# Kernel tuning notes

Hardware: AMD Instinct MI355X
Metric: run time of the kernel (lower is better)

The kernel has to match this reference:

```python
import jax, jax.numpy as jnp
import numpy as np

B, S, D = 4, 4096, 1024
H, DK, DV = 8, 128, 128
SEG = 512
DH = 4096
EPS = 1e-5


def setup_inputs() -> dict:
    key = jax.random.key(0)
    ks = jax.random.split(key, 8)
    n = lambda k, shp, sc: (jax.random.normal(k, shp, jnp.float32) * sc)
    return {
        "x": n(ks[0], (B, S, D), 1.0),
        "ln_gamma": jnp.ones((D,), jnp.float32),
        "ln_beta": jnp.zeros((D,), jnp.float32),
        "Wq": n(ks[1], (D, H * DK), 0.02),
        "Wk": n(ks[2], (D, H * DK), 0.02),
        "Wv": n(ks[3], (D, H * DV), 0.02),
        "Wo": n(ks[4], (H * DV, D), 0.02),
        "betas": n(ks[5], (1, H, 1, DV), 1.0),
        "ff_w1": n(ks[6], (D, DH), 0.02),
        "ff_b1": jnp.zeros((DH,), jnp.float32),
        "ff_w2": n(ks[7], (DH, D), 0.02),
        "ff_b2": jnp.zeros((D,), jnp.float32),
    }


def layer_norm(x, gamma, beta):
    mu = x.mean(-1, keepdims=True)
    var = x.var(-1, keepdims=True)
    return (x - mu) * jax.lax.rsqrt(var + EPS) * gamma + beta


def gelu_tanh(x):
    c = np.sqrt(2.0 / np.pi).astype(np.float32)
    return 0.5 * x * (1.0 + jnp.tanh(c * (x + 0.044715 * x * x * x)))


def infini_attention(x, Wq, Wk, Wv, Wo, betas):
    b, s, _ = x.shape
    nseg = s // SEG

    def proj(W, dh):
        # (b,s,H*dh) -> (nseg, b, H, SEG, dh)
        y = (x @ W).reshape(b, nseg, SEG, H, dh)
        return y.transpose(1, 0, 3, 2, 4)

    q = proj(Wq, DK)
    k = proj(Wk, DK)
    v = proj(Wv, DV)

    gate = jax.nn.sigmoid(betas)  # (1,H,1,DV)
    scale = 1.0 / np.sqrt(DK).astype(np.float32)
    causal_mask = jnp.tril(jnp.ones((SEG, SEG), bool))

    def step(carry, qkv):
        mem, z = carry  # (b,H,DK,DV), (b,H,DK,1)
        qs, ks_, vs = qkv  # (b,H,SEG,dk/dv)
        sq = jax.nn.elu(qs) + 1.0
        # compressive-memory retrieval
        att_mem = (sq @ mem) / (sq @ z)  # (b,H,SEG,DV)
        # local (segment) dot-product attention
        scores = jnp.einsum("bhqk,bhsk->bhqs", qs, ks_) * scale
        scores = jnp.where(causal_mask, scores, -jnp.inf)
        att = jax.nn.softmax(scores, axis=-1) @ vs  # (b,H,SEG,DV)
        # linear memory update
        sk = jax.nn.elu(ks_) + 1.0
        mem = mem + jnp.einsum("bhsk,bhsv->bhkv", sk, vs)
        z = z + sk.sum(axis=2)[..., None]
        out = gate * att_mem + (1.0 - gate) * att
        return (mem, z), out

    mem0 = jnp.zeros((b, H, DK, DV), x.dtype)
    z0 = jnp.ones((b, H, DK, 1), x.dtype) / DK
    _, outs = jax.lax.scan(step, (mem0, z0), (q, k, v))
    # (nseg,b,H,SEG,DV) -> (b,s,H*DV)
    outs = outs.transpose(1, 0, 3, 2, 4).reshape(b, s, H * DV)
    return outs @ Wo


def reference(x, ln_gamma, ln_beta, Wq, Wk, Wv, Wo, betas, ff_w1, ff_b1, ff_w2, ff_b2):
    h = layer_norm(x, ln_gamma, ln_beta)
    x = x + infini_attention(h, Wq, Wk, Wv, Wo, betas)
    h = layer_norm(x, ln_gamma, ln_beta)
    ff = gelu_tanh(h @ ff_w1 + ff_b1) @ ff_w2 + ff_b2
    return x + ff
```

## Files before the change

kernel.cpp:

```cpp
#include <hip/hip_runtime.h>

typedef unsigned short u16;
typedef unsigned int   u32;
typedef float f32x4 __attribute__((ext_vector_type(4)));
typedef short bf16x8 __attribute__((ext_vector_type(8)));

#define DEV static __device__ __forceinline__

DEV u16 f2b(float f){
  u32 u = __builtin_bit_cast(u32, f);
  return (u16)((u + 0x7fffu + ((u >> 16) & 1u)) >> 16);
}
DEV float b2f(u16 h){ u32 u = ((u32)h) << 16; return __builtin_bit_cast(float, u); }
DEV u32 pack2(float a, float b){ return (u32)f2b(a) | ((u32)f2b(b) << 16); }
DEV uint4 pack8(const float* f){
  uint4 r; r.x = pack2(f[0],f[1]); r.y = pack2(f[2],f[3]);
  r.z = pack2(f[4],f[5]); r.w = pack2(f[6],f[7]); return r;
}
DEV void unpack8(uint4 u, float* f){
  f[0]=b2f((u16)(u.x&0xffffu)); f[1]=b2f((u16)(u.x>>16));
  f[2]=b2f((u16)(u.y&0xffffu)); f[3]=b2f((u16)(u.y>>16));
  f[4]=b2f((u16)(u.z&0xffffu)); f[5]=b2f((u16)(u.z>>16));
  f[6]=b2f((u16)(u.w&0xffffu)); f[7]=b2f((u16)(u.w>>16));
}
DEV float gelu_t(float x){
  return 0.5f*x*(1.f + tanhf(0.7978845608028654f*(x + 0.044715f*x*x*x)));
}
DEV void g2l16(const u16* g, u16* l){
  __builtin_amdgcn_global_load_lds(
    (const __attribute__((address_space(1))) u32*)g,
    (__attribute__((address_space(3))) u32*)l, 16, 0, 0);
}

__global__ __launch_bounds__(256)
void ln_k(const float* __restrict__ x, const float* __restrict__ gamma,
          const float* __restrict__ beta, u16* __restrict__ out)
{
  const int row = blockIdx.x;
  const int t = threadIdx.x;
  const float4 v = ((const float4*)(x + (size_t)row*1024))[t];
  float s  = v.x+v.y+v.z+v.w;
  float ss = v.x*v.x+v.y*v.y+v.z*v.z+v.w*v.w;
  #pragma unroll
  for (int o=32;o;o>>=1){ s += __shfl_xor(s,o); ss += __shfl_xor(ss,o); }
  __shared__ float rs[4], rq[4];
  if ((t&63)==0){ rs[t>>6]=s; rq[t>>6]=ss; }
  __syncthreads();
  s  = rs[0]+rs[1]+rs[2]+rs[3];
  ss = rq[0]+rq[1]+rq[2]+rq[3];
  const float mean = s*(1.f/1024.f);
  const float var  = ss*(1.f/1024.f) - mean*mean;
  const float inv  = rsqrtf(var + 1e-5f);
  const float4 g4 = ((const float4*)gamma)[t];
  const float4 b4 = ((const float4*)beta)[t];
  float o[4];
  o[0]=(v.x-mean)*inv*g4.x+b4.x; o[1]=(v.y-mean)*inv*g4.y+b4.y;
  o[2]=(v.z-mean)*inv*g4.z+b4.z; o[3]=(v.w-mean)*inv*g4.w+b4.w;
  uint2 w; w.x = pack2(o[0],o[1]); w.y = pack2(o[2],o[3]);
  *(uint2*)(out + (size_t)row*1024 + t*4) = w;
}

__global__ __launch_bounds__(256)
void wconv_k(const float* __restrict__ W, u16* __restrict__ WT, int K, int N)
{
  __shared__ float tile[32][33];
  const int k0 = blockIdx.y<<5, n0 = blockIdx.x<<5;
  const int tx = threadIdx.x & 31, ty = threadIdx.x >> 5;
  #pragma unroll
  for (int r=0;r<32;r+=8)
    tile[ty+r][tx] = W[(size_t)(k0+ty+r)*N + n0+tx];
  __syncthreads();
  #pragma unroll
  for (int r=0;r<32;r+=8)
    WT[(size_t)(n0+ty+r)*K + k0+tx] = f2b(tile[tx][ty+r]);
}

#define EPI_QKV  0
#define EPI_WO   1
#define EPI_GELU 2
#define EPI_FF2  3

template<int EPI>
__global__ __launch_bounds__(512)
void gemm3_k(const u16* __restrict__ A, const u16* __restrict__ BT,
             int K, int lda, int ldb, int N,
             u16* __restrict__ obf, float* __restrict__ of32,
             const float* __restrict__ res, const float* __restrict__ bias)
{
  __shared__ __align__(16) u16 SA[2*4096];
  __shared__ __align__(16) u16 SB[2*8192];
  const int t = threadIdx.x, wid = t>>6, lane = t&63;
  const int c = lane&15, g = lane>>4;
  const int wm = wid>>2, wn = wid&3;
  const int nwg = gridDim.x*gridDim.y;
  const int lb = blockIdx.y*gridDim.x + blockIdx.x;
  const int nl = (lb&7)*(nwg>>3) + (lb>>3);
  const int bx = nl % gridDim.x, by = nl / gridDim.x;
  const int m0 = by<<7, n0 = bx<<8;
  const int srow = lane>>2;
  const int scol = (lane&3)<<3;
  const int sxor = (srow&3)<<3;
  const int rowA = (wid<<4) + srow;
  const u16* aSrc  = A  + (size_t)(m0 + rowA)*lda + (scol ^ sxor);
  const u16* bSrc0 = BT + (size_t)(n0 + rowA)*ldb + (scol ^ sxor);
  const u16* bSrc1 = BT + (size_t)(n0 + 128 + rowA)*ldb + (scol ^ sxor);
  const int kx = (g<<3) ^ ((c&3)<<3);

  f32x4 acc[4][4];
  const f32x4 zz = {0.f,0.f,0.f,0.f};
  #pragma unroll
  for (int i=0;i<4;i++){ acc[i][0]=zz; acc[i][1]=zz; acc[i][2]=zz; acc[i][3]=zz; }

  g2l16(aSrc,  &SA[wid<<9]);
  g2l16(bSrc0, &SB[wid<<9]);
  g2l16(bSrc1, &SB[(wid<<9) + 4096]);
  __syncthreads();

  const int nt = K >> 5;
  for (int tt = 0; tt < nt; ++tt){
    const int cur = tt & 1;
    if (tt + 1 < nt){
      const int ko = (tt+1) << 5;
      g2l16(aSrc + ko,  &SA[((cur^1)<<12) + (wid<<9)]);
      g2l16(bSrc0 + ko, &SB[((cur^1)<<13) + (wid<<9)]);
      g2l16(bSrc1 + ko, &SB[((cur^1)<<13) + (wid<<9) + 4096]);
    }
    bf16x8 af[4], bf[4];
    #pragma unroll
    for (int i=0;i<4;i++)
      af[i] = *(const bf16x8*)&SA[(cur<<12) + ((wm<<6)+(i<<4)+c)*32 + kx];
    #pragma unroll
    for (int j=0;j<4;j++)
      bf[j] = *(const bf16x8*)&SB[(cur<<13) + ((wn<<6)+(j<<4)+c)*32 + kx];
    #pragma unroll
    for (int i=0;i<4;i++)
      #pragma unroll
      for (int j=0;j<4;j++)
        acc[i][j] = __builtin_amdgcn_mfma_f32_16x16x32_bf16(af[i], bf[j], acc[i][j], 0,0,0);
    __syncthreads();
  }

  #pragma unroll
  for (int i=0;i<4;i++){
    const int gr0 = m0 + (wm<<6) + (i<<4) + (g<<2);
    #pragma unroll
    for (int j=0;j<4;j++){
      const int gc = n0 + (wn<<6) + (j<<4) + c;
      #pragma unroll
      for (int r=0;r<4;r++){
        const int gr = gr0 + r;
        const float vv = acc[i][j][r];
        if (EPI==EPI_QKV){
          obf[((size_t)(gc>>10)<<24) + (size_t)gr*1024 + (gc&1023)] = f2b(vv);
        } else if (EPI==EPI_WO){
          const size_t idx = (size_t)gr*N + gc;
          of32[idx] = res[idx] + vv;
        } else if (EPI==EPI_GELU){
          obf[(size_t)gr*N + gc] = f2b(gelu_t(vv + bias[gc]));
        } else {
          const size_t idx = (size_t)gr*N + gc;
          of32[idx] = of32[idx] + vv + (bias ? bias[gc] : 0.f);
        }
      }
    }
  }
}

__global__ __launch_bounds__(256)
void memseg_k(const u16* __restrict__ kb, const u16* __restrict__ vb,
              float* __restrict__ Mseg, float* __restrict__ zseg)
{
  const int bid = blockIdx.x;
  const int seg = bid & 7, h = (bid>>3)&7, b = bid>>6;
  __shared__ __align__(16) u16 Kt[128*64];
  __shared__ __align__(16) u16 Vt[128*64];
  const int t=threadIdx.x, w=t>>6, lane=t&63, c=lane&15, g=lane>>4;

  f32x4 acc[2][8];
  f32x4 zacc[2];
  const f32x4 zzero = {0.f,0.f,0.f,0.f};
  #pragma unroll
  for (int d=0;d<2;d++){ zacc[d]=zzero;
    #pragma unroll
    for (int j=0;j<8;j++) acc[d][j]=zzero; }
  bf16x8 bones;
  { u16 tmp[8];
    #pragma unroll
    for (int e=0;e<8;e++) tmp[e] = (c==0) ? (u16)0x3F80 : (u16)0;
    bones = __builtin_bit_cast(bf16x8, *(uint4*)tmp); }

  for (int s0=0; s0<512; s0+=64){
    __syncthreads();
    {
      const int s = lane, dk0 = w<<5;
      const size_t grow = ((size_t)b*4096 + seg*512 + s0 + s)*1024 + h*128 + dk0;
      #pragma unroll
      for (int jj=0;jj<4;jj++){
        float kf[8], vf[8];
        unpack8(*(const uint4*)(kb + grow + jj*8), kf);
        unpack8(*(const uint4*)(vb + grow + jj*8), vf);
        #pragma unroll
        for (int e=0;e<8;e++){
          const int dk = dk0 + jj*8 + e;
          const float ek = kf[e]>0.f ? kf[e]+1.f : __expf(kf[e]);
          Kt[(dk<<6) + (s ^ ((dk&7)<<3))] = f2b(ek);
          Vt[(dk<<6) + (s ^ ((dk&7)<<3))] = f2b(vf[e]);
        }
      }
    }
    __syncthreads();
    #pragma unroll
    for (int ks=0;ks<2;ks++){
      const int kc = (ks<<5) + (g<<3);
      const bf16x8 a0 = *(const bf16x8*)&Kt[((((w<<1)  )*16 + c)<<6) + (kc ^ ((c&7)<<3))];
      const bf16x8 a1 = *(const bf16x8*)&Kt[((((w<<1)+1)*16 + c)<<6) + (kc ^ ((c&7)<<3))];
      zacc[0] = __builtin_amdgcn_mfma_f32_16x16x32_bf16(a0, bones, zacc[0], 0,0,0);
      zacc[1] = __builtin_amdgcn_mfma_f32_16x16x32_bf16(a1, bones, zacc[1], 0,0,0);
      #pragma unroll
      for (int j=0;j<8;j++){
        const bf16x8 bv = *(const bf16x8*)&Vt[(((j<<4) + c)<<6) + (kc ^ ((c&7)<<3))];
        acc[0][j] = __builtin_amdgcn_mfma_f32_16x16x32_bf16(a0, bv, acc[0][j], 0,0,0);
        acc[1][j] = __builtin_amdgcn_mfma_f32_16x16x32_bf16(a1, bv, acc[1][j], 0,0,0);
      }
    }
  }
  const size_t mb = (size_t)bid*16384;
  #pragma unroll
  for (int d=0;d<2;d++){
    const int dk = ((w<<1)+d)*16 + (g<<2);
    #pragma unroll
    for (int j=0;j<8;j++)
      #pragma unroll
      for (int r=0;r<4;r++)
        Mseg[mb + (size_t)(dk + r)*128 + (j<<4) + c] = acc[d][j][r];
    if (c==0){
      #pragma unroll
      for (int r=0;r<4;r++) zseg[(size_t)bid*128 + dk + r] = zacc[d][r];
    }
  }
}

__global__ __launch_bounds__(256)
void scan_k(const float* __restrict__ Mseg, const float* __restrict__ zseg,
            u16* __restrict__ memBT, float* __restrict__ zB)
{
  const int bh = blockIdx.x >> 3, oct = blockIdx.x & 7;
  const int t = threadIdx.x;
  const int dv = (oct<<4) + (t&15);
  const int kd0 = (t>>4)<<3;
  float run[8];
  #pragma unroll
  for (int i=0;i<8;i++) run[i]=0.f;
  for (int seg=0; seg<8; seg++){
    const size_t base = ((size_t)bh*8 + seg)*16384;
    u16 tmp[8];
    #pragma unroll
    for (int i=0;i<8;i++) tmp[i] = f2b(run[i]);
    *(uint4*)(memBT + base + (size_t)dv*128 + kd0) = *(const uint4*)tmp;
    #pragma unroll
    for (int i=0;i<8;i++) run[i] += Mseg[base + (size_t)(kd0+i)*128 + dv];
  }
  if (oct==0 && t < 128){
    float zr = 1.f/128.f;
    for (int seg=0; seg<8; seg++){
      const size_t base = ((size_t)bh*8 + seg)*128;
      zB[base + t] = zr;
      zr += zseg[base + t];
    }
  }
}

__global__ __launch_bounds__(256,4)
void attn_k(const u16* __restrict__ qb, const u16* __restrict__ kb,
            const u16* __restrict__ vb, const u16* __restrict__ memBT,
            const float* __restrict__ zB, const float* __restrict__ betas,
            u16* __restrict__ attc)
{
  const int bid = blockIdx.x;
  const int s = bid & 255, rt = 7 - (bid >> 8);
  const int seg = s&7, h=(s>>3)&7, b=s>>6;
  __shared__ __align__(16) u16 smem[16384];
  __shared__ __align__(16) u16 Ps[4096];
  u16* Ks = smem;
  u16* Vt = smem + 8192;
  float* zP = (float*)Ps;
  const int t=threadIdx.x, w=t>>6, lane=t&63, c=lane&15, g=lane>>4;
  const size_t base = ((size_t)b*4096 + seg*512)*1024 + h*128;

  bf16x8 af[4];
  {
    const u16* qsrc = qb + base + (size_t)(rt*64 + (w<<4) + c)*1024 + (g<<3);
    #pragma unroll
    for (int ks=0;ks<4;ks++) af[ks] = *(const bf16x8*)(qsrc + ks*32);
  }
  f32x4 acc[8];
  #pragma unroll
  for (int f=0;f<8;f++) acc[f] = (f32x4){0.f,0.f,0.f,0.f};
  float m_run[4], l_run[4];
  #pragma unroll
  for (int r=0;r<4;r++){ m_run[r] = -1e30f; l_run[r] = 0.f; }
  const float scl = 0.08838834764831845f;

  for (int kc=0; kc<=rt; kc++){
    __syncthreads();
    #pragma unroll
    for (int j=0;j<4;j++){
      const int row = (j<<2) + (lane>>4);
      const u16* src = kb + base + (size_t)(kc*64 + (w<<4) + row)*1024
                       + ((size_t)((lane&15) ^ (((w<<4)+row)&7)) << 3);
      g2l16(src, Ks + (((w<<4)+(j<<2))<<7));
    }
    {
      const int kr = lane, d0 = w<<5;
      const u16* vsrc = vb + base + (size_t)(kc*64+kr)*1024 + d0;
      #pragma unroll
      for (int jj=0;jj<4;jj++){
        const uint4 vv = *(const uint4*)(vsrc + jj*8);
        u16 tmp[8]; *(uint4*)tmp = vv;
        #pragma unroll
        for (int e=0;e<8;e++){
          const int dv = d0 + jj*8 + e;
          Vt[(dv<<6) + (kr ^ ((dv&7)<<3))] = tmp[e];
        }
      }
    }
    __syncthreads();
    f32x4 sv[4];
    #pragma unroll
    for (int j=0;j<4;j++) sv[j] = (f32x4){0.f,0.f,0.f,0.f};
    #pragma unroll
    for (int ks=0;ks<4;ks++)
      #pragma unroll
      for (int j=0;j<4;j++){
        const bf16x8 bk = *(const bf16x8*)&Ks[(((j<<4)+c)<<7) + ((((ks<<2)|g) ^ (c&7))<<3)];
        sv[j] = __builtin_amdgcn_mfma_f32_16x16x32_bf16(af[ks], bk, sv[j], 0,0,0);
      }
    const bool diag = (kc==rt);
    float p[4][4], rm[4], rsum[4];
    #pragma unroll
    for (int r=0;r<4;r++){
      float mx = -1e30f;
      #pragma unroll
      for (int j=0;j<4;j++){
        float svv = sv[j][r]*scl;
        if (diag && ((j<<4)+c) > ((w<<4) + (g<<2) + r)) svv = -1e30f;
        p[j][r] = svv;
        mx = fmaxf(mx, svv);
      }
      rm[r] = mx;
    }
    #pragma unroll
    for (int o=1;o<16;o<<=1)
      #pragma unroll
      for (int r=0;r<4;r++) rm[r] = fmaxf(rm[r], __shfl_xor(rm[r], o));
    #pragma unroll
    for (int r=0;r<4;r++){
      const float mn = fmaxf(m_run[r], rm[r]);
      const float sc = __expf(m_run[r] - mn);
      m_run[r] = mn;
      float sum = 0.f;
      #pragma unroll
      for (int j=0;j<4;j++){ p[j][r] = __expf(p[j][r]-mn); sum += p[j][r]; }
      rsum[r] = sum;
      l_run[r] *= sc;
      #pragma unroll
      for (int f=0;f<8;f++) acc[f][r] *= sc;
    }
    #pragma unroll
    for (int o=1;o<16;o<<=1)
      #pragma unroll
      for (int r=0;r<4;r++) rsum[r] += __shfl_xor(rsum[r], o);
    #pragma unroll
    for (int r=0;r<4;r++) l_run[r] += rsum[r];
    #pragma unroll
    for (int j=0;j<4;j++)
      #pragma unroll
      for (int r=0;r<4;r++){
        const int prow = (w<<4)+(g<<2)+r;
        Ps[(prow<<6) + (((j<<4)+c) ^ ((prow&7)<<3))] = f2b(p[j][r]);
      }
    #pragma unroll
    for (int ks2=0; ks2<2; ks2++){
      const bf16x8 pa = *(const bf16x8*)&Ps[(((w<<4)+c)<<6) + ((((ks2<<2)|g) ^ (c&7))<<3)];
      #pragma unroll
      for (int f=0;f<8;f++){
        const int dv = (f<<4)+c;
        const bf16x8 bv = *(const bf16x8*)&Vt[(dv<<6) + ((((ks2<<2)|g) ^ (c&7))<<3)];
        acc[f] = __builtin_amdgcn_mfma_f32_16x16x32_bf16(pa, bv, acc[f], 0,0,0);
      }
    }
  }
  __syncthreads();
  {
    const size_t mbase = (((size_t)b*8+h)*8+seg) << 14;
    #pragma unroll
    for (int i=0;i<8;i++){
      const int row = (i<<2) + (lane>>4);
      const u16* src = memBT + mbase + ((size_t)((w<<5)+row)<<7)
                       + ((size_t)((lane&15) ^ (((w<<5)+row)&7)) << 3);
      g2l16(src, smem + (((w<<5)+(i<<2))<<7));
    }
    if (t < 128) zP[t] = zB[((((size_t)b*8+h)*8+seg)<<7) + t];
  }
  __syncthreads();
  bf16x8 af2[4];
  #pragma unroll
  for (int ks=0;ks<4;ks++){
    float f[8]; unpack8(__builtin_bit_cast(uint4, af[ks]), f);
    #pragma unroll
    for (int e=0;e<8;e++) f[e] = f[e]>0.f ? f[e]+1.f : __expf(f[e]);
    af2[ks] = __builtin_bit_cast(bf16x8, pack8(f));
  }
  bf16x8 bz[4];
  #pragma unroll
  for (int ks=0;ks<4;ks++){
    uint4 zr = {0,0,0,0};
    if (c==0) zr = pack8(&zP[ks*32 + (g<<3)]);
    bz[ks] = __builtin_bit_cast(bf16x8, zr);
  }
  f32x4 nacc[8];
  f32x4 zacc = {0.f,0.f,0.f,0.f};
  #pragma unroll
  for (int f=0;f<8;f++) nacc[f] = zacc;
  #pragma unroll
  for (int ks=0;ks<4;ks++){
    zacc = __builtin_amdgcn_mfma_f32_16x16x32_bf16(af2[ks], bz[ks], zacc, 0,0,0);
    #pragma unroll
    for (int f=0;f<8;f++){
      const bf16x8 bm = *(const bf16x8*)&smem[(((f<<4)+c)<<7) + ((((ks<<2)|g) ^ (c&7))<<3)];
      nacc[f] = __builtin_amdgcn_mfma_f32_16x16x32_bf16(af2[ks], bm, nacc[f], 0,0,0);
    }
  }
  float den[4];
  #pragma unroll
  for (int r=0;r<4;r++) den[r] = 1.f / __shfl(zacc[r], lane & 48);
  #pragma unroll
  for (int f=0;f<8;f++){
    const float bv = betas[(h<<7) + (f<<4) + c];
    const float gate = 1.f/(1.f+__expf(-bv));
    #pragma unroll
    for (int r=0;r<4;r++){
      const size_t idx = base + (size_t)(rt*64 + (w<<4) + (g<<2) + r)*1024 + (f<<4) + c;
      const float att = acc[f][r] / l_run[r];
      const float am  = nacc[f][r] * den[r];
      attc[idx] = f2b(gate*am + (1.f-gate)*att);
    }
  }
}

extern "C" void kernel_launch(void* const* d_in, const int* in_sizes, int n_in,
                              void* d_out, int out_size, void* d_ws, size_t ws_size,
                              hipStream_t stream)
{
  (void)in_sizes; (void)n_in; (void)out_size; (void)ws_size;
  const float* x    = (const float*)d_in[0];
  const float* ln_g = (const float*)d_in[1];
  const float* ln_b = (const float*)d_in[2];
  const float* Wq   = (const float*)d_in[3];
  const float* Wk   = (const float*)d_in[4];
  const float* Wv   = (const float*)d_in[5];
  const float* Wo   = (const float*)d_in[6];
  const float* betas= (const float*)d_in[7];
  const float* w1   = (const float*)d_in[8];
  const float* b1   = (const float*)d_in[9];
  const float* w2   = (const float*)d_in[10];
  const float* b2   = (const float*)d_in[11];
  float* out = (float*)d_out;

  char* ws = (char*)d_ws;
  const size_t MB = 1048576;
  u16* qb  = (u16*)(ws);
  u16* kb  = (u16*)(ws + 32*MB);
  u16* vb  = (u16*)(ws + 64*MB);
  u16* Wqkv= (u16*)(ws + 96*MB);
  u16* Wob = (u16*)(ws + 102*MB);
  u16* w1b = (u16*)(ws + 104*MB);
  u16* w2b = (u16*)(ws + 112*MB);
  char* ob = (char*)d_out;
  u16*   h    = (u16*)ob;
  float* Mseg = (float*)(ob + 32*MB);
  u16*   memBT= (u16*)  (ob + 48*MB);
  float* zseg = (float*)(ob + 56*MB);
  float* zB   = (float*)(ob + 56*MB + 131072);
  u16*   at   = qb;
  u16*   h2   = kb;
  u16*   gb   = vb;

  wconv_k<<<dim3(32,32),256,0,stream>>>(Wq, Wqkv,              1024,1024);
  wconv_k<<<dim3(32,32),256,0,stream>>>(Wk, Wqkv+1024*1024,    1024,1024);
  wconv_k<<<dim3(32,32),256,0,stream>>>(Wv, Wqkv+2*1024*1024,  1024,1024);
  wconv_k<<<dim3(32,32),256,0,stream>>>(Wo, Wob, 1024,1024);
  wconv_k<<<dim3(128,32),256,0,stream>>>(w1, w1b, 1024,4096);
  wconv_k<<<dim3(32,128),256,0,stream>>>(w2, w2b, 4096,1024);

  ln_k<<<16384,256,0,stream>>>(x, ln_g, ln_b, h);
  gemm3_k<EPI_QKV><<<dim3(12,128),512,0,stream>>>(h, Wqkv, 1024,1024,1024, 3072,
                                                  qb, nullptr, nullptr, nullptr);
  memseg_k<<<256,256,0,stream>>>(kb, vb, Mseg, zseg);
  scan_k<<<256,256,0,stream>>>(Mseg, zseg, memBT, zB);
  attn_k<<<2048,256,0,stream>>>(qb, kb, vb, memBT, zB, betas, at);
  gemm3_k<EPI_WO><<<dim3(4,128),512,0,stream>>>(at, Wob, 1024,1024,1024, 1024,
                                                nullptr, out, x, nullptr);
  ln_k<<<16384,256,0,stream>>>(out, ln_g, ln_b, h2);
  for (int cc = 0; cc < 4; cc++){
    gemm3_k<EPI_GELU><<<dim3(4,128),512,0,stream>>>(h2, w1b + (size_t)cc*1024*1024,
                                                    1024,1024,1024, 1024,
                                                    gb, nullptr, nullptr, b1 + cc*1024);
    gemm3_k<EPI_FF2><<<dim3(4,128),512,0,stream>>>(gb, w2b + (size_t)cc*1024,
                                                   1024,1024,4096, 1024,
                                                   nullptr, out, nullptr,
                                                   cc==0 ? b2 : nullptr);
  }
}
```

Baseline: 832.7 us.

## Restructure attention to one block per segment with balanced causal query tiles

The attention kernel now launches one 512-thread block per (batch, head, segment) instead of eight 256-thread blocks per segment. Each wave owns two 32-row query tiles chosen as w and 15-w, so causal work is balanced across waves. K and V are staged once per key chunk into double-buffered shared memory, with the next chunk prefetched while the current one is computed, and output is written back through shared memory as coalesced 16-byte stores. This cuts the repeated K/V global loads across row-tile blocks, but it drops to 256 blocks at one block per CU, with much higher register and LDS use per block.

```diff
diff --git a/kernel.cpp b/kernel.cpp
--- a/kernel.cpp
+++ b/kernel.cpp
@@ -270,182 +270,216 @@
   }
 }
 
-__global__ __launch_bounds__(256,4)
+__global__ __launch_bounds__(512,1)
 void attn_k(const u16* __restrict__ qb, const u16* __restrict__ kb,
             const u16* __restrict__ vb, const u16* __restrict__ memBT,
             const float* __restrict__ zB, const float* __restrict__ betas,
             u16* __restrict__ attc)
 {
-  const int bid = blockIdx.x;
-  const int s = bid & 255, rt = 7 - (bid >> 8);
+  const int s = blockIdx.x;
   const int seg = s&7, h=(s>>3)&7, b=s>>6;
-  __shared__ __align__(16) u16 smem[16384];
-  __shared__ __align__(16) u16 Ps[4096];
-  u16* Ks = smem;
-  u16* Vt = smem + 8192;
-  float* zP = (float*)Ps;
+  __shared__ __align__(16) u16 KV[32768];
+  __shared__ __align__(16) u16 WS[8][4096];
+  __shared__ float zsl[128];
   const int t=threadIdx.x, w=t>>6, lane=t&63, c=lane&15, g=lane>>4;
   const size_t base = ((size_t)b*4096 + seg*512)*1024 + h*128;
-
-  bf16x8 af[4];
-  {
-    const u16* qsrc = qb + base + (size_t)(rt*64 + (w<<4) + c)*1024 + (g<<3);
-    #pragma unroll
-    for (int ks=0;ks<4;ks++) af[ks] = *(const bf16x8*)(qsrc + ks*32);
-  }
-  f32x4 acc[8];
-  #pragma unroll
-  for (int f=0;f<8;f++) acc[f] = (f32x4){0.f,0.f,0.f,0.f};
-  float m_run[4], l_run[4];
-  #pragma unroll
-  for (int r=0;r<4;r++){ m_run[r] = -1e30f; l_run[r] = 0.f; }
+  const int qtA = w, qtB = 15-w;
+  u16* WSw = &WS[w][0];
   const float scl = 0.08838834764831845f;
 
-  for (int kc=0; kc<=rt; kc++){
-    __syncthreads();
-    #pragma unroll
-    for (int j=0;j<4;j++){
-      const int row = (j<<2) + (lane>>4);
-      const u16* src = kb + base + (size_t)(kc*64 + (w<<4) + row)*1024
-                       + ((size_t)((lane&15) ^ (((w<<4)+row)&7)) << 3);
-      g2l16(src, Ks + (((w<<4)+(j<<2))<<7));
-    }
-    {
-      const int kr = lane, d0 = w<<5;
-      const u16* vsrc = vb + base + (size_t)(kc*64+kr)*1024 + d0;
-      #pragma unroll
-      for (int jj=0;jj<4;jj++){
-        const uint4 vv = *(const uint4*)(vsrc + jj*8);
-        u16 tmp[8]; *(uint4*)tmp = vv;
-        #pragma unroll
-        for (int e=0;e<8;e++){
-          const int dv = d0 + jj*8 + e;
-          Vt[(dv<<6) + (kr ^ ((dv&7)<<3))] = tmp[e];
-        }
-      }
-    }
-    __syncthreads();
-    f32x4 sv[4];
-    #pragma unroll
-    for (int j=0;j<4;j++) sv[j] = (f32x4){0.f,0.f,0.f,0.f};
+  bf16x8 qA0[4], qA1[4], qB0[4], qB1[4];
+  #pragma unroll
+  for (int ks=0;ks<4;ks++){
+    qA0[ks] = *(const bf16x8*)(qb + base + (size_t)(qtA*32 +      c)*1024 + ks*32 + (g<<3));
+    qA1[ks] = *(const bf16x8*)(qb + base + (size_t)(qtA*32 + 16 + c)*1024 + ks*32 + (g<<3));
+    qB0[ks] = *(const bf16x8*)(qb + base + (size_t)(qtB*32 +      c)*1024 + ks*32 + (g<<3));
+    qB1[ks] = *(const bf16x8*)(qb + base + (size_t)(qtB*32 + 16 + c)*1024 + ks*32 + (g<<3));
+  }
+  f32x4 aA0[8], aA1[8], aB0[8], aB1[8];
+  #pragma unroll
+  for (int f=0;f<8;f++){
+    aA0[f]=(f32x4){0,0,0,0}; aA1[f]=(f32x4){0,0,0,0};
+    aB0[f]=(f32x4){0,0,0,0}; aB1[f]=(f32x4){0,0,0,0};
+  }
+  float m[16], l[16];
+  #pragma unroll
+  for (int i=0;i<16;i++){ m[i]=-1e30f; l[i]=0.f; }
+
+  uint4 vv0, vv1;
+  #define STAGE_K(kc, buf) { \
+    _Pragma("unroll") \
+    for (int j2=0;j2<2;j2++){ \
+      const int row = (w<<3) + (j2<<2) + (lane>>4); \
+      const u16* src = kb + base + (size_t)((kc)*64 + row)*1024 \
+                       + ((size_t)((lane&15) ^ (row&7)) << 3); \
+      g2l16(src, KV + (buf)*16384 + (((w<<3)+(j2<<2))<<7)); } }
+  #define STAGE_V_LOAD(kc) { \
+    const u16* vsrc = vb + base + (size_t)((kc)*64 + lane)*1024 + (w<<4); \
+    vv0 = *(const uint4*)(vsrc); vv1 = *(const uint4*)(vsrc + 8); }
+  #define STAGE_V_WRITE(buf) { \
+    u16 tmpv[16]; *(uint4*)tmpv = vv0; *(uint4*)(tmpv+8) = vv1; \
+    _Pragma("unroll") \
+    for (int e=0;e<16;e++){ const int dv = (w<<4)+e; \
+      KV[(buf)*16384 + 8192 + (dv<<6) + (lane ^ ((dv&7)<<3))] = tmpv[e]; } }
+
+  auto frag_step = [&](f32x4 (&S)[4], f32x4 (&A)[8], float* mm, float* ll,
+                       int rowbase, bool diag, int kc, const u16* Vt, u16* Pfr){
+    float p[4][4], rm[4], rs[4];
+    #pragma unroll
+    for (int r=0;r<4;r++){
+      float mx = -1e30f;
+      #pragma unroll
+      for (int j=0;j<4;j++){
+        float v = S[j][r]*scl;
+        if (diag && (kc*64 + (j<<4)+c) > (rowbase + (g<<2)+r)) v = -1e30f;
+        p[j][r]=v; mx=fmaxf(mx,v);
+      }
+      rm[r]=mx;
+    }
+    #pragma unroll
+    for (int o=1;o<16;o<<=1)
+      #pragma unroll
+      for (int r=0;r<4;r++) rm[r]=fmaxf(rm[r], __shfl_xor(rm[r],o));
+    #pragma unroll
+    for (int r=0;r<4;r++){
+      const float mn = fmaxf(mm[r], rm[r]);
+      const float sc = __expf(mm[r]-mn);
+      mm[r]=mn;
+      float sum=0.f;
+      #pragma unroll
+      for (int j=0;j<4;j++){ p[j][r]=__expf(p[j][r]-mn); sum+=p[j][r]; }
+      rs[r]=sum; ll[r]*=sc;
+      #pragma unroll
+      for (int f=0;f<8;f++) A[f][r]*=sc;
+    }
+    #pragma unroll
+    for (int o=1;o<16;o<<=1)
+      #pragma unroll
+      for (int r=0;r<4;r++) rs[r]+=__shfl_xor(rs[r],o);
+    #pragma unroll
+    for (int r=0;r<4;r++) ll[r]+=rs[r];
+    #pragma unroll
+    for (int j=0;j<4;j++)
+      #pragma unroll
+      for (int r=0;r<4;r++){
+        const int pr = (g<<2)+r;
+        Pfr[(pr<<6) + (((j<<4)+c) ^ ((pr&7)<<3))] = f2b(p[j][r]);
+      }
+    #pragma unroll
+    for (int ks2=0;ks2<2;ks2++){
+      const bf16x8 pa = *(const bf16x8*)&Pfr[(c<<6) + ((((ks2<<2)|g) ^ (c&7))<<3)];
+      #pragma unroll
+      for (int f=0;f<8;f++){
+        const bf16x8 bv = *(const bf16x8*)&Vt[(((f<<4)+c)<<6) + ((((ks2<<2)|g) ^ (c&7))<<3)];
+        A[f] = __builtin_amdgcn_mfma_f32_16x16x32_bf16(pa, bv, A[f], 0,0,0);
+      }
+    }
+  };
+  auto do_qt = [&](const bf16x8 (&Q0)[4], const bf16x8 (&Q1)[4],
+                   f32x4 (&A0)[8], f32x4 (&A1)[8], float* mm, float* ll,
+                   int qt, int kc, const u16* Ks, const u16* Vt){
+    f32x4 s0[4], s1[4];
+    #pragma unroll
+    for (int j=0;j<4;j++){ s0[j]=(f32x4){0,0,0,0}; s1[j]=(f32x4){0,0,0,0}; }
     #pragma unroll
     for (int ks=0;ks<4;ks++)
       #pragma unroll
       for (int j=0;j<4;j++){
         const bf16x8 bk = *(const bf16x8*)&Ks[(((j<<4)+c)<<7) + ((((ks<<2)|g) ^ (c&7))<<3)];
-        sv[j] = __builtin_amdgcn_mfma_f32_16x16x32_bf16(af[ks], bk, sv[j], 0,0,0);
-      }
-    const bool diag = (kc==rt);
-    float p[4][4], rm[4], rsum[4];
-    #pragma unroll
-    for (int r=0;r<4;r++){
-      float mx = -1e30f;
-      #pragma unroll
-      for (int j=0;j<4;j++){
-        float svv = sv[j][r]*scl;
-        if (diag && ((j<<4)+c) > ((w<<4) + (g<<2) + r)) svv = -1e30f;
-        p[j][r] = svv;
-        mx = fmaxf(mx, svv);
-      }
-      rm[r] = mx;
-    }
-    #pragma unroll
-    for (int o=1;o<16;o<<=1)
-      #pragma unroll
-      for (int r=0;r<4;r++) rm[r] = fmaxf(rm[r], __shfl_xor(rm[r], o));
-    #pragma unroll
-    for (int r=0;r<4;r++){
-      const float mn = fmaxf(m_run[r], rm[r]);
-      const float sc = __expf(m_run[r] - mn);
-      m_run[r] = mn;
-      float sum = 0.f;
-      #pragma unroll
-      for (int j=0;j<4;j++){ p[j][r] = __expf(p[j][r]-mn); sum += p[j][r]; }
-      rsum[r] = sum;
-      l_run[r] *= sc;
-      #pragma unroll
-      for (int f=0;f<8;f++) acc[f][r] *= sc;
-    }
-    #pragma unroll
-    for (int o=1;o<16;o<<=1)
-      #pragma unroll
-      for (int r=0;r<4;r++) rsum[r] += __shfl_xor(rsum[r], o);
-    #pragma unroll
-    for (int r=0;r<4;r++) l_run[r] += rsum[r];
-    #pragma unroll
-    for (int j=0;j<4;j++)
+        s0[j] = __builtin_amdgcn_mfma_f32_16x16x32_bf16(Q0[ks], bk, s0[j], 0,0,0);
+        s1[j] = __builtin_amdgcn_mfma_f32_16x16x32_bf16(Q1[ks], bk, s1[j], 0,0,0);
+      }
+    const bool diag = (kc == (qt>>1));
+    frag_step(s0, A0, mm,   ll,   qt*32,      diag, kc, Vt, WSw);
+    frag_step(s1, A1, mm+4, ll+4, qt*32 + 16, diag, kc, Vt, WSw + 1024);
+  };
+
+  STAGE_K(0, 0);
+  STAGE_V_LOAD(0); STAGE_V_WRITE(0);
+  if (t < 128) zsl[t] = zB[((((size_t)b*8+h)*8+seg)<<7) + t];
+  __syncthreads();
+
+  for (int kc=0; kc<8; ++kc){
+    const int cur = kc & 1;
+    if (kc+1 < 8){
+      STAGE_K(kc+1, cur^1);
+      STAGE_V_LOAD(kc+1);
+    } else {
+      const size_t mbase = (((size_t)b*8+h)*8+seg) << 14;
+      #pragma unroll
+      for (int j2=0;j2<4;j2++){
+        const int row = (w<<4) + (j2<<2) + (lane>>4);
+        const u16* src = memBT + mbase + ((size_t)row<<7)
+                         + ((size_t)((lane&15) ^ (row&7)) << 3);
+        g2l16(src, KV + (((w<<4)+(j2<<2))<<7));
+      }
+    }
+    const u16* Ks = KV + cur*16384;
+    const u16* Vt = KV + cur*16384 + 8192;
+    if (kc <= (qtA>>1)) do_qt(qA0, qA1, aA0, aA1, m,   l,   qtA, kc, Ks, Vt);
+    if (kc <= (qtB>>1)) do_qt(qB0, qB1, aB0, aB1, m+8, l+8, qtB, kc, Ks, Vt);
+    if (kc+1 < 8) STAGE_V_WRITE(cur^1);
+    __syncthreads();
+  }
+
+  auto epi_frag = [&](const bf16x8 (&Qf)[4], f32x4 (&A)[8], float* ll, u16* outb){
+    bf16x8 af2[4];
+    #pragma unroll
+    for (int ks=0;ks<4;ks++){
+      float f[8]; unpack8(__builtin_bit_cast(uint4, Qf[ks]), f);
+      #pragma unroll
+      for (int e=0;e<8;e++) f[e] = f[e]>0.f ? f[e]+1.f : __expf(f[e]);
+      af2[ks] = __builtin_bit_cast(bf16x8, pack8(f));
+    }
+    bf16x8 bz[4];
+    #pragma unroll
+    for (int ks=0;ks<4;ks++){
+      uint4 zr = {0,0,0,0};
+      if (c==0) zr = pack8(&zsl[ks*32 + (g<<3)]);
+      bz[ks] = __builtin_bit_cast(bf16x8, zr);
+    }
+    f32x4 zacc = {0,0,0,0};
+    f32x4 nacc[8];
+    #pragma unroll
+    for (int f=0;f<8;f++) nacc[f]=(f32x4){0,0,0,0};
+    #pragma unroll
+    for (int ks=0;ks<4;ks++){
+      zacc = __builtin_amdgcn_mfma_f32_16x16x32_bf16(af2[ks], bz[ks], zacc, 0,0,0);
+      #pragma unroll
+      for (int f=0;f<8;f++){
+        const bf16x8 bm = *(const bf16x8*)&KV[(((f<<4)+c)<<7) + ((((ks<<2)|g) ^ (c&7))<<3)];
+        nacc[f] = __builtin_amdgcn_mfma_f32_16x16x32_bf16(af2[ks], bm, nacc[f], 0,0,0);
+      }
+    }
+    float den[4];
+    #pragma unroll
+    for (int r=0;r<4;r++) den[r] = 1.f/__shfl(zacc[r], lane & 48);
+    #pragma unroll
+    for (int f=0;f<8;f++){
+      const float bv = betas[(h<<7) + (f<<4) + c];
+      const float gate = 1.f/(1.f+__expf(-bv));
       #pragma unroll
       for (int r=0;r<4;r++){
-        const int prow = (w<<4)+(g<<2)+r;
-        Ps[(prow<<6) + (((j<<4)+c) ^ ((prow&7)<<3))] = f2b(p[j][r]);
-      }
-    #pragma unroll
-    for (int ks2=0; ks2<2; ks2++){
-      const bf16x8 pa = *(const bf16x8*)&Ps[(((w<<4)+c)<<6) + ((((ks2<<2)|g) ^ (c&7))<<3)];
-      #pragma unroll
-      for (int f=0;f<8;f++){
-        const int dv = (f<<4)+c;
-        const bf16x8 bv = *(const bf16x8*)&Vt[(dv<<6) + ((((ks2<<2)|g) ^ (c&7))<<3)];
-        acc[f] = __builtin_amdgcn_mfma_f32_16x16x32_bf16(pa, bv, acc[f], 0,0,0);
-      }
-    }
-  }
-  __syncthreads();
-  {
-    const size_t mbase = (((size_t)b*8+h)*8+seg) << 14;
-    #pragma unroll
-    for (int i=0;i<8;i++){
-      const int row = (i<<2) + (lane>>4);
-      const u16* src = memBT + mbase + ((size_t)((w<<5)+row)<<7)
-                       + ((size_t)((lane&15) ^ (((w<<5)+row)&7)) << 3);
-      g2l16(src, smem + (((w<<5)+(i<<2))<<7));
-    }
-    if (t < 128) zP[t] = zB[((((size_t)b*8+h)*8+seg)<<7) + t];
-  }
-  __syncthreads();
-  bf16x8 af2[4];
-  #pragma unroll
-  for (int ks=0;ks<4;ks++){
-    float f[8]; unpack8(__builtin_bit_cast(uint4, af[ks]), f);
-    #pragma unroll
-    for (int e=0;e<8;e++) f[e] = f[e]>0.f ? f[e]+1.f : __expf(f[e]);
-    af2[ks] = __builtin_bit_cast(bf16x8, pack8(f));
-  }
-  bf16x8 bz[4];
-  #pragma unroll
-  for (int ks=0;ks<4;ks++){
-    uint4 zr = {0,0,0,0};
-    if (c==0) zr = pack8(&zP[ks*32 + (g<<3)]);
-    bz[ks] = __builtin_bit_cast(bf16x8, zr);
-  }
-  f32x4 nacc[8];
-  f32x4 zacc = {0.f,0.f,0.f,0.f};
-  #pragma unroll
-  for (int f=0;f<8;f++) nacc[f] = zacc;
-  #pragma unroll
-  for (int ks=0;ks<4;ks++){
-    zacc = __builtin_amdgcn_mfma_f32_16x16x32_bf16(af2[ks], bz[ks], zacc, 0,0,0);
-    #pragma unroll
-    for (int f=0;f<8;f++){
-      const bf16x8 bm = *(const bf16x8*)&smem[(((f<<4)+c)<<7) + ((((ks<<2)|g) ^ (c&7))<<3)];
-      nacc[f] = __builtin_amdgcn_mfma_f32_16x16x32_bf16(af2[ks], bm, nacc[f], 0,0,0);
-    }
-  }
-  float den[4];
-  #pragma unroll
-  for (int r=0;r<4;r++) den[r] = 1.f / __shfl(zacc[r], lane & 48);
-  #pragma unroll
-  for (int f=0;f<8;f++){
-    const float bv = betas[(h<<7) + (f<<4) + c];
-    const float gate = 1.f/(1.f+__expf(-bv));
-    #pragma unroll
-    for (int r=0;r<4;r++){
-      const size_t idx = base + (size_t)(rt*64 + (w<<4) + (g<<2) + r)*1024 + (f<<4) + c;
-      const float att = acc[f][r] / l_run[r];
-      const float am  = nacc[f][r] * den[r];
-      attc[idx] = f2b(gate*am + (1.f-gate)*att);
-    }
-  }
+        const int rl = (g<<2)+r;
+        const float att = A[f][r]/ll[r];
+        const float am  = nacc[f][r]*den[r];
+        outb[(rl<<7) + (((f<<4)+c) ^ ((rl&7)<<3))] = f2b(gate*am + (1.f-gate)*att);
+      }
+    }
+  };
+  #define WRITE_QT(qt) { \
+    _Pragma("unroll") \
+    for (int i=0;i<8;i++){ \
+      const int row = (i<<2) + (lane>>4); \
+      const uint4 v = *(const uint4*)&WSw[(row<<7) + (((c<<3)) ^ ((row&7)<<3))]; \
+      *(uint4*)(attc + base + (size_t)((qt)*32 + row)*1024 + (c<<3)) = v; } }
+
+  epi_frag(qA0, aA0, l,    WSw);
+  epi_frag(qA1, aA1, l+4,  WSw + 2048);
+  WRITE_QT(qtA);
+  epi_frag(qB0, aB0, l+8,  WSw);
+  epi_frag(qB1, aB1, l+12, WSw + 2048);
+  WRITE_QT(qtB);
 }
 
 extern "C" void kernel_launch(void* const* d_in, const int* in_sizes, int n_in,
@@ -498,7 +532,7 @@
                                                   qb, nullptr, nullptr, nullptr);
   memseg_k<<<256,256,0,stream>>>(kb, vb, Mseg, zseg);
   scan_k<<<256,256,0,stream>>>(Mseg, zseg, memBT, zB);
-  attn_k<<<2048,256,0,stream>>>(qb, kb, vb, memBT, zB, betas, at);
+  attn_k<<<256,512,0,stream>>>(qb, kb, vb, memBT, zB, betas, at);
   gemm3_k<EPI_WO><<<dim3(4,128),512,0,stream>>>(at, Wob, 1024,1024,1024, 1024,
                                                 nullptr, out, x, nullptr);
   ln_k<<<16384,256,0,stream>>>(out, ln_g, ln_b, h2);
```

After: 1.005 ms. +20.7%, slower.
